# Kernel optimization log

Measured on AMD Instinct MI355X. Metric: run time of the kernel, lower is better.

The kernel has to match this reference:

```python
import jax, jax.numpy as jnp
import numpy as np

B, S, E = 2, 2048, 2048
H, G = 16, 4
HD = E // H          # 128
GD = HD * G          # 512
NGH = H // G         # 4 (tile factor for K/V heads)


def setup_inputs() -> dict:
    key = jax.random.key(0)
    ks = jax.random.split(key, 6)
    sc = 0.02
    return {
        "x": jax.random.normal(ks[0], (B, S, E), dtype=jnp.float32),
        "mask": jnp.ones((B, S, S), dtype=jnp.int32),
        "Wq": jax.random.normal(ks[1], (E, E), dtype=jnp.float32) * sc,
        "bq": jnp.zeros((E,), dtype=jnp.float32),
        "Wk": jax.random.normal(ks[2], (E, GD), dtype=jnp.float32) * sc,
        "bk": jnp.zeros((GD,), dtype=jnp.float32),
        "Wv": jax.random.normal(ks[3], (E, GD), dtype=jnp.float32) * sc,
        "bv": jnp.zeros((GD,), dtype=jnp.float32),
        "Wo": jax.random.normal(ks[4], (E, E), dtype=jnp.float32) * sc,
        "bo": jnp.zeros((E,), dtype=jnp.float32),
    }


def reference(x, mask, Wq, bq, Wk, bk, Wv, bv, Wo, bo):
    b, s, _ = x.shape
    # projections
    q = x @ Wq + bq                                   # [B,S,E]
    k = x @ Wk + bk                                   # [B,S,GD]
    v = x @ Wv + bv                                   # [B,S,GD]
    q = q.reshape(b, s, H, HD).transpose(0, 2, 1, 3)  # [B,H,S,hd]
    k = k.reshape(b, s, G, HD).transpose(0, 2, 1, 3)  # [B,G,S,hd]
    v = v.reshape(b, s, G, HD).transpose(0, 2, 1, 3)
    # torch .repeat(1, NGH, 1, 1): tile groups -> head h uses group h % G
    k = jnp.tile(k, (1, NGH, 1, 1))                   # [B,H,S,hd]
    v = jnp.tile(v, (1, NGH, 1, 1))
    scale = 1.0 / np.sqrt(HD).astype(np.float32)
    scores = jnp.einsum("bhqd,bhkd->bhqk", q, k) * scale
    m = mask[:, None, :, :]                           # [B,1,S,S]
    scores = jnp.where(m == 0, jnp.float32(-10000.0), scores)
    attn = jax.nn.softmax(scores, axis=-1)
    out = jnp.einsum("bhqk,bhkd->bhqd", attn, v)      # [B,H,S,hd]
    out = out.transpose(0, 2, 1, 3).reshape(b, s, E)  # [B,S,E]
    return out @ Wo + bo
```

## Files before the change

kernel.cpp:

```cpp
#include <hip/hip_runtime.h>

#define B_ 2
#define S_ 2048
#define E_ 2048
#define H_ 16
#define G_ 4
#define HD_ 128
#define GD_ 512
#define KVLD_ 1024
#define QKVN_ 3072
#define M_ (B_*S_)

using u16 = unsigned short;
using u32 = unsigned int;
typedef __attribute__((ext_vector_type(8))) short short8;
typedef __attribute__((ext_vector_type(4))) float f32x4;

#define QSCL 0.12751891114f
#define MASKED_L2 (-14427.0f)

__device__ __forceinline__ u16 f2bf(float f) {
  union { float f; unsigned u; } v; v.f = f;
  unsigned r = v.u + 0x7fff + ((v.u >> 16) & 1);
  return (u16)(r >> 16);
}

__device__ __forceinline__ void async16(const void* g, void* l) {
  __builtin_amdgcn_global_load_lds((const __attribute__((address_space(1))) unsigned int*)g,
                                   (__attribute__((address_space(3))) unsigned int*)l, 16, 0, 0);
}

__global__ __launch_bounds__(256) void cast_f32_bf16(const float* __restrict__ in,
                                                     u16* __restrict__ out, int n4) {
  int i = blockIdx.x * 256 + threadIdx.x;
  if (i >= n4) return;
  float4 v = ((const float4*)in)[i];
  union { u16 o[4]; uint2 u; } pk;
  pk.o[0] = f2bf(v.x); pk.o[1] = f2bf(v.y); pk.o[2] = f2bf(v.z); pk.o[3] = f2bf(v.w);
  *(uint2*)(out + (size_t)i * 4) = pk.u;
}

__global__ __launch_bounds__(256) void concat_bias3(const float* __restrict__ a,
                                                    const float* __restrict__ b,
                                                    const float* __restrict__ c,
                                                    float* __restrict__ o) {
  int t = blockIdx.x * 256 + threadIdx.x;
  if (t < 2048) o[t] = a[t];
  else if (t < 2560) o[t] = b[t - 2048];
  else if (t < 3072) o[t] = c[t - 2560];
}

__global__ __launch_bounds__(256) void transpose_cast(const float* __restrict__ W,
                                                      u16* __restrict__ Wt, int K, int N) {
  __shared__ u16 tile[64 * 72];
  int n0 = blockIdx.x * 64, k0 = blockIdx.y * 64;
  int t = threadIdx.x;
  int row = t >> 2;
  int seg = t & 3;
  const float* src = W + (size_t)(k0 + row) * N + n0 + seg * 16;
  #pragma unroll
  for (int i = 0; i < 4; ++i) {
    float4 v = *(const float4*)(src + i * 4);
    int nl = seg * 16 + i * 4;
    tile[(nl + 0) * 72 + row] = f2bf(v.x);
    tile[(nl + 1) * 72 + row] = f2bf(v.y);
    tile[(nl + 2) * 72 + row] = f2bf(v.z);
    tile[(nl + 3) * 72 + row] = f2bf(v.w);
  }
  __syncthreads();
  int nl = t >> 2, s2 = t & 3;
  u16* dst = Wt + (size_t)(n0 + nl) * K + k0 + s2 * 16;
  *(uint4*)dst       = *(const uint4*)&tile[nl * 72 + s2 * 16];
  *(uint4*)(dst + 8) = *(const uint4*)&tile[nl * 72 + s2 * 16 + 8];
}

__global__ __launch_bounds__(256) void transpose_v(const u16* __restrict__ KVb, u16* __restrict__ Vtg) {
  __shared__ u16 tile[64 * 72];
  int kv0 = blockIdx.x * 64;
  int gn0 = blockIdx.y * 64;
  int t = threadIdx.x;
  int row = t >> 2, seg = t & 3;
  int prow = (row & 15) * 4 + (row >> 4);
  const u16* src = KVb + (size_t)(kv0 + row) * KVLD_ + 512 + gn0 + seg * 16;
  union { uint4 v; u16 s[8]; } a, b;
  a.v = *(const uint4*)src; b.v = *(const uint4*)(src + 8);
  #pragma unroll
  for (int j = 0; j < 8; ++j) tile[(seg * 16 + j) * 72 + prow] = a.s[j];
  #pragma unroll
  for (int j = 0; j < 8; ++j) tile[(seg * 16 + 8 + j) * 72 + prow] = b.s[j];
  __syncthreads();
  int gl = t >> 2, ks2 = t & 3;
  int bb = kv0 >> 11;
  int s0 = kv0 & 2047;
  int gn = gn0 + gl;
  u16* dst = Vtg + (size_t)(bb * 512 + gn) * S_ + s0 + ks2 * 16;
  *(uint4*)dst       = *(const uint4*)&tile[gl * 72 + ks2 * 16];
  *(uint4*)(dst + 8) = *(const uint4*)&tile[gl * 72 + ks2 * 16 + 8];
}

__global__ __launch_bounds__(256) void mask_flags(const int* __restrict__ mask, int* __restrict__ flags) {
  int idx = blockIdx.x * 4 + (threadIdx.x >> 6);
  int lane = threadIdx.x & 63;
  int bb = idx >> 12, rg = (idx >> 5) & 127, kt = idx & 31;
  const int* base = mask + ((size_t)bb * S_ + rg * 16) * S_ + kt * 64;
  int row = lane >> 2, c0 = (lane & 3) * 16;
  int ok = 1;
  #pragma unroll
  for (int i = 0; i < 4; ++i) {
    int4 v = *(const int4*)&base[(size_t)row * S_ + c0 + i * 4];
    ok &= (v.x != 0) & (v.y != 0) & (v.z != 0) & (v.w != 0);
  }
  ok = __all(ok) ? 1 : 0;
  if (lane == 0) flags[idx] = ok;
}

__global__ __launch_bounds__(256) void gemm_qkv(const u16* __restrict__ A, const u16* __restrict__ Bt,
                                                const float* __restrict__ bias,
                                                u16* __restrict__ Qb, u16* __restrict__ KVb, int K) {
  __shared__ u16 As[128 * 32];
  __shared__ u16 Bs[128 * 32];
  int nbx = gridDim.x;
  int bid = blockIdx.y * nbx + blockIdx.x;
  int chunk = (nbx * gridDim.y) >> 3;
  int swz = (bid & 7) * chunk + (bid >> 3);
  int n0 = (swz % nbx) * 128, m0 = (swz / nbx) * 128;
  int t = threadIdx.x;
  int w = t >> 6, lane = t & 63, c = lane & 15, q = lane >> 4;
  int wm = w & 1, wn = w >> 1;
  int r0 = t >> 2, kc = t & 3;
  const u16* Ag0 = A  + (size_t)(m0 + r0) * K + kc * 8;
  const u16* Ag1 = A  + (size_t)(m0 + 64 + r0) * K + kc * 8;
  const u16* Bg0 = Bt + (size_t)(n0 + r0) * K + kc * 8;
  const u16* Bg1 = Bt + (size_t)(n0 + 64 + r0) * K + kc * 8;
  f32x4 acc[4][4] = {};
  for (int k0 = 0; k0 < K; k0 += 32) {
    async16(Ag0 + k0, &As[t * 8]);
    async16(Ag1 + k0, &As[2048 + t * 8]);
    async16(Bg0 + k0, &Bs[t * 8]);
    async16(Bg1 + k0, &Bs[2048 + t * 8]);
    __syncthreads();
    short8 af[4], bf[4];
    #pragma unroll
    for (int i = 0; i < 4; ++i) {
      af[i] = *(const short8*)&As[(wm * 64 + i * 16 + c) * 32 + q * 8];
      bf[i] = *(const short8*)&Bs[(wn * 64 + i * 16 + c) * 32 + q * 8];
    }
    #pragma unroll
    for (int i = 0; i < 4; ++i)
      #pragma unroll
      for (int j = 0; j < 4; ++j)
        acc[i][j] = __builtin_amdgcn_mfma_f32_16x16x32_bf16(af[i], bf[j], acc[i][j], 0, 0, 0);
    __syncthreads();
  }
  int isq = (n0 < 2048);
  #pragma unroll
  for (int i = 0; i < 4; ++i) {
    int mrow_base = m0 + wm * 64 + i * 16 + q * 4;
    #pragma unroll
    for (int j = 0; j < 4; ++j) {
      int coln = n0 + wn * 64 + j * 16 + c;
      float bv = bias[coln];
      #pragma unroll
      for (int r = 0; r < 4; ++r) {
        float v = acc[i][j][r] + bv;
        if (isq) Qb[(size_t)(mrow_base + r) * E_ + coln] = f2bf(v * QSCL);
        else     KVb[(size_t)(mrow_base + r) * KVLD_ + coln - 2048] = f2bf(v);
      }
    }
  }
}

__global__ __launch_bounds__(256) void gemm_k(const u16* __restrict__ A, const u16* __restrict__ Bt,
                                              const float* __restrict__ bias, float* __restrict__ Cout,
                                              int M, int N, int K) {
  __shared__ u16 As[128 * 32];
  __shared__ u16 Bs[128 * 32];
  int nbx = gridDim.x;
  int bid = blockIdx.y * nbx + blockIdx.x;
  int chunk = (nbx * gridDim.y) >> 3;
  int swz = (bid & 7) * chunk + (bid >> 3);
  int n0 = (swz % nbx) * 128, m0 = (swz / nbx) * 128;
  int t = threadIdx.x;
  int w = t >> 6, lane = t & 63, c = lane & 15, q = lane >> 4;
  int wm = w & 1, wn = w >> 1;
  int r0 = t >> 2, kc = t & 3;
  const u16* Ag0 = A  + (size_t)(m0 + r0) * K + kc * 8;
  const u16* Ag1 = A  + (size_t)(m0 + 64 + r0) * K + kc * 8;
  const u16* Bg0 = Bt + (size_t)(n0 + r0) * K + kc * 8;
  const u16* Bg1 = Bt + (size_t)(n0 + 64 + r0) * K + kc * 8;
  f32x4 acc[4][4] = {};
  for (int k0 = 0; k0 < K; k0 += 32) {
    async16(Ag0 + k0, &As[t * 8]);
    async16(Ag1 + k0, &As[2048 + t * 8]);
    async16(Bg0 + k0, &Bs[t * 8]);
    async16(Bg1 + k0, &Bs[2048 + t * 8]);
    __syncthreads();
    short8 af[4], bf[4];
    #pragma unroll
    for (int i = 0; i < 4; ++i) {
      af[i] = *(const short8*)&As[(wm * 64 + i * 16 + c) * 32 + q * 8];
      bf[i] = *(const short8*)&Bs[(wn * 64 + i * 16 + c) * 32 + q * 8];
    }
    #pragma unroll
    for (int i = 0; i < 4; ++i)
      #pragma unroll
      for (int j = 0; j < 4; ++j)
        acc[i][j] = __builtin_amdgcn_mfma_f32_16x16x32_bf16(af[i], bf[j], acc[i][j], 0, 0, 0);
    __syncthreads();
  }
  #pragma unroll
  for (int i = 0; i < 4; ++i) {
    int mrow_base = m0 + wm * 64 + i * 16 + q * 4;
    #pragma unroll
    for (int j = 0; j < 4; ++j) {
      int coln = n0 + wn * 64 + j * 16 + c;
      float bv = bias[coln];
      #pragma unroll
      for (int r = 0; r < 4; ++r)
        Cout[(size_t)(mrow_base + r) * N + coln] = acc[i][j][r] + bv;
    }
  }
}

__global__ __launch_bounds__(512) void attn_k(const u16* __restrict__ Q, const u16* __restrict__ KVb,
                                              const u16* __restrict__ Vtg, const int* __restrict__ mask,
                                              const int* __restrict__ mflags, u16* __restrict__ O) {
  __shared__ u16 Ks[2][64 * 128];
  __shared__ u16 Vs[2][128 * 64];
  __shared__ u16 Ps[8 * 16 * 64];
  int bid = blockIdx.x;
  int mt = bid & 15, h = (bid >> 4) & 15, bb = bid >> 8;
  int g = h & 3;
  int t = threadIdx.x, w = t >> 6, lane = t & 63, c = lane & 15, q = lane >> 4;
  int m0 = mt * 128;

  const u16* Qbase  = Q   + (size_t)(bb * S_ + m0) * E_ + h * HD_;
  const u16* Kbase  = KVb + (size_t)bb * S_ * KVLD_ + g * HD_;
  const u16* Vtbase = Vtg + (size_t)(bb * G_ + g) * HD_ * S_;

  int krow0 = t >> 4;
  int kkc   = ((t & 15) ^ (krow0 & 15)) * 8;
  const u16* Kst = Kbase + (size_t)krow0 * KVLD_ + kkc;
  int vn0 = t >> 3;
  int vkc = ((t & 7) ^ (vn0 & 7)) * 8;
  const u16* Vst = Vtbase + (size_t)vn0 * S_ + vkc;

  int pwa[4], pra[2];
  #pragma unroll
  for (int r = 0; r < 4; ++r) {
    int row = q * 4 + r;
    pwa[r] = w * 1024 + row * 64 + (((c >> 1) ^ (row & 7)) * 8) + (c & 1) * 4;
  }
  #pragma unroll
  for (int ks = 0; ks < 2; ++ks)
    pra[ks] = w * 1024 + c * 64 + (((ks * 4 + q) ^ (c & 7)) * 8);

  short8 aq[4];
  #pragma unroll
  for (int k0 = 0; k0 < 4; ++k0)
    aq[k0] = *(const short8*)&Qbase[(size_t)(w * 16 + c) * E_ + k0 * 32 + q * 8];

  const short8 ones = {(short)0x3F80, (short)0x3F80, (short)0x3F80, (short)0x3F80,
                       (short)0x3F80, (short)0x3F80, (short)0x3F80, (short)0x3F80};

  f32x4 Oa[8] = {};
  f32x4 lacc = {};

  #pragma unroll
  for (int p = 0; p < 2; ++p)
    async16(Kst + (size_t)(p * 32) * KVLD_, &Ks[0][p * 4096 + t * 8]);
  #pragma unroll
  for (int p = 0; p < 2; ++p)
    async16(Vst + (size_t)(p * 64) * S_, &Vs[0][p * 4096 + t * 8]);

  for (int kv0 = 0; kv0 < S_; kv0 += 64) {
    int cur = (kv0 >> 6) & 1;
    __syncthreads();
    if (kv0 + 64 < S_) {
      #pragma unroll
      for (int p = 0; p < 2; ++p)
        async16(Kst + (size_t)(kv0 + 64 + p * 32) * KVLD_, &Ks[cur ^ 1][p * 4096 + t * 8]);
      #pragma unroll
      for (int p = 0; p < 2; ++p)
        async16(Vst + (size_t)(p * 64) * S_ + kv0 + 64, &Vs[cur ^ 1][p * 4096 + t * 8]);
    }
    const u16* K_ = Ks[cur];
    const u16* V_ = Vs[cur];

    f32x4 sc[4] = {};
    #pragma unroll
    for (int k0 = 0; k0 < 4; ++k0) {
      short8 bk[4];
      #pragma unroll
      for (int ns = 0; ns < 4; ++ns)
        bk[ns] = *(const short8*)&K_[(ns * 16 + c) * 128 + (((k0 * 4 + q) ^ c) * 8)];
      #pragma unroll
      for (int ns = 0; ns < 4; ++ns)
        sc[ns] = __builtin_amdgcn_mfma_f32_16x16x32_bf16(aq[k0], bk[ns], sc[ns], 0, 0, 0);
    }
    {
      int flag = mflags[bb * 4096 + (mt * 8 + w) * 32 + (kv0 >> 6)];
      if (!flag) {
        #pragma unroll
        for (int r = 0; r < 4; ++r) {
          int qrow = m0 + w * 16 + q * 4 + r;
          const int* mrow = mask + ((size_t)bb * S_ + qrow) * S_ + kv0;
          #pragma unroll
          for (int ns = 0; ns < 4; ++ns)
            if (mrow[ns * 16 + c] == 0) sc[ns][r] = MASKED_L2;
        }
      }
    }
    #pragma unroll
    for (int r = 0; r < 4; ++r) {
      u32 u[4];
      #pragma unroll
      for (int ns = 0; ns < 4; ++ns) {
        float p = __builtin_amdgcn_exp2f(sc[ns][r]);
        u[ns] = __float_as_uint(p) + 0x8000u;
      }
      uint2 pk;
      pk.x = __builtin_amdgcn_perm(u[1], u[0], 0x07060302);
      pk.y = __builtin_amdgcn_perm(u[3], u[2], 0x07060302);
      *(uint2*)&Ps[pwa[r]] = pk;
    }
    __asm__ volatile("" ::: "memory");
    #pragma unroll
    for (int ks = 0; ks < 2; ++ks) {
      short8 ap = *(const short8*)&Ps[pra[ks]];
      lacc = __builtin_amdgcn_mfma_f32_16x16x32_bf16(ap, ones, lacc, 0, 0, 0);
      #pragma unroll
      for (int d = 0; d < 8; ++d) {
        short8 bv = *(const short8*)&V_[(d * 16 + c) * 64 + (((ks * 4 + q) ^ (c & 7)) * 8)];
        Oa[d] = __builtin_amdgcn_mfma_f32_16x16x32_bf16(ap, bv, Oa[d], 0, 0, 0);
      }
    }
  }
  {
    float inv[4];
    #pragma unroll
    for (int r = 0; r < 4; ++r) inv[r] = 1.0f / lacc[r];
    #pragma unroll
    for (int d = 0; d < 8; ++d)
      #pragma unroll
      for (int r = 0; r < 4; ++r) {
        size_t off = (size_t)(bb * S_ + m0 + w * 16 + q * 4 + r) * E_ + h * HD_ + d * 16 + c;
        O[off] = f2bf(Oa[d][r] * inv[r]);
      }
  }
}

extern "C" void kernel_launch(void* const* d_in, const int* in_sizes, int n_in,
                              void* d_out, int out_size, void* d_ws, size_t ws_size,
                              hipStream_t stream) {
  const float* x    = (const float*)d_in[0];
  const int*   mask = (const int*)d_in[1];
  const float* Wq   = (const float*)d_in[2];
  const float* bq   = (const float*)d_in[3];
  const float* Wk   = (const float*)d_in[4];
  const float* bk   = (const float*)d_in[5];
  const float* Wv   = (const float*)d_in[6];
  const float* bv   = (const float*)d_in[7];
  const float* Wo   = (const float*)d_in[8];
  const float* bo   = (const float*)d_in[9];
  float* out = (float*)d_out;

  char* ws = (char*)d_ws;
  u16* xb    = (u16*)ws; ws += (size_t)M_ * E_ * 2;
  u16* Wqkvt = (u16*)ws; ws += (size_t)QKVN_ * E_ * 2;
  u16* Wot   = (u16*)ws; ws += (size_t)E_ * E_ * 2;
  u16* Qb    = (u16*)ws; ws += (size_t)M_ * E_ * 2;
  u16* KVb   = (u16*)ws; ws += (size_t)M_ * KVLD_ * 2;
  u16* Ob    = (u16*)ws; ws += (size_t)M_ * E_ * 2;
  u16* Vtg   = (u16*)ws; ws += (size_t)B_ * G_ * HD_ * S_ * 2;
  int* mfl   = (int*)ws; ws += (size_t)B_ * 128 * 32 * 4;
  float* bqkv = (float*)ws; ws += QKVN_ * 4;

  cast_f32_bf16<<<(M_ * E_ / 4 + 255) / 256, 256, 0, stream>>>(x, xb, M_ * E_ / 4);
  transpose_cast<<<dim3(E_ / 64,  E_ / 64), 256, 0, stream>>>(Wq, Wqkvt, E_, E_);
  transpose_cast<<<dim3(GD_ / 64, E_ / 64), 256, 0, stream>>>(Wk, Wqkvt + (size_t)2048 * E_, E_, GD_);
  transpose_cast<<<dim3(GD_ / 64, E_ / 64), 256, 0, stream>>>(Wv, Wqkvt + (size_t)2560 * E_, E_, GD_);
  transpose_cast<<<dim3(E_ / 64,  E_ / 64), 256, 0, stream>>>(Wo, Wot, E_, E_);
  concat_bias3<<<QKVN_ / 256, 256, 0, stream>>>(bq, bk, bv, bqkv);
  mask_flags<<<B_ * 128 * 32 / 4, 256, 0, stream>>>(mask, mfl);

  gemm_qkv<<<dim3(QKVN_ / 128, M_ / 128), 256, 0, stream>>>(xb, Wqkvt, bqkv, Qb, KVb, E_);
  transpose_v<<<dim3(M_ / 64, GD_ / 64), 256, 0, stream>>>(KVb, Vtg);

  attn_k<<<B_ * H_ * (S_ / 128), 512, 0, stream>>>(Qb, KVb, Vtg, mask, mfl, Ob);

  gemm_k<<<dim3(E_ / 128, M_ / 128), 256, 0, stream>>>(Ob, Wot, bo, out, M_, E_, E_);
}
```

Baseline: 362.8 us.

## Double-buffer LDS tiles and XOR-swizzle chunks in both GEMM kernels

Both the QKV projection GEMM and the output GEMM now use two LDS buffers. The next K-slice is prefetched asynchronously while MFMAs run on the current one, and the second barrier per iteration is dropped. The 16-byte chunk layout within each LDS row is also XOR-swizzled by row, on both the store and the read side, to cut bank conflicts on the fragment loads. This doubles LDS use per block, which could reduce occupancy, and the overlap depends on how the async copies are waited on at the barrier.

```diff
diff --git a/kernel.cpp b/kernel.cpp
--- a/kernel.cpp
+++ b/kernel.cpp
@@ -117,8 +117,8 @@
 __global__ __launch_bounds__(256) void gemm_qkv(const u16* __restrict__ A, const u16* __restrict__ Bt,
                                                 const float* __restrict__ bias,
                                                 u16* __restrict__ Qb, u16* __restrict__ KVb, int K) {
-  __shared__ u16 As[128 * 32];
-  __shared__ u16 Bs[128 * 32];
+  __shared__ u16 As[2][128 * 32];
+  __shared__ u16 Bs[2][128 * 32];
   int nbx = gridDim.x;
   int bid = blockIdx.y * nbx + blockIdx.x;
   int chunk = (nbx * gridDim.y) >> 3;
@@ -127,30 +127,38 @@
   int t = threadIdx.x;
   int w = t >> 6, lane = t & 63, c = lane & 15, q = lane >> 4;
   int wm = w & 1, wn = w >> 1;
-  int r0 = t >> 2, kc = t & 3;
-  const u16* Ag0 = A  + (size_t)(m0 + r0) * K + kc * 8;
-  const u16* Ag1 = A  + (size_t)(m0 + 64 + r0) * K + kc * 8;
-  const u16* Bg0 = Bt + (size_t)(n0 + r0) * K + kc * 8;
-  const u16* Bg1 = Bt + (size_t)(n0 + 64 + r0) * K + kc * 8;
+  int r0 = t >> 2;
+  int kcs = ((t & 3) ^ ((t >> 3) & 3)) * 8;
+  const u16* Ag0 = A  + (size_t)(m0 + r0) * K + kcs;
+  const u16* Ag1 = A  + (size_t)(m0 + 64 + r0) * K + kcs;
+  const u16* Bg0 = Bt + (size_t)(n0 + r0) * K + kcs;
+  const u16* Bg1 = Bt + (size_t)(n0 + 64 + r0) * K + kcs;
+  int roff = (q ^ ((c >> 1) & 3)) * 8;
   f32x4 acc[4][4] = {};
+  async16(Ag0, &As[0][t * 8]);
+  async16(Ag1, &As[0][2048 + t * 8]);
+  async16(Bg0, &Bs[0][t * 8]);
+  async16(Bg1, &Bs[0][2048 + t * 8]);
   for (int k0 = 0; k0 < K; k0 += 32) {
-    async16(Ag0 + k0, &As[t * 8]);
-    async16(Ag1 + k0, &As[2048 + t * 8]);
-    async16(Bg0 + k0, &Bs[t * 8]);
-    async16(Bg1 + k0, &Bs[2048 + t * 8]);
+    int cur = (k0 >> 5) & 1;
     __syncthreads();
+    if (k0 + 32 < K) {
+      async16(Ag0 + k0 + 32, &As[cur ^ 1][t * 8]);
+      async16(Ag1 + k0 + 32, &As[cur ^ 1][2048 + t * 8]);
+      async16(Bg0 + k0 + 32, &Bs[cur ^ 1][t * 8]);
+      async16(Bg1 + k0 + 32, &Bs[cur ^ 1][2048 + t * 8]);
+    }
     short8 af[4], bf[4];
     #pragma unroll
     for (int i = 0; i < 4; ++i) {
-      af[i] = *(const short8*)&As[(wm * 64 + i * 16 + c) * 32 + q * 8];
-      bf[i] = *(const short8*)&Bs[(wn * 64 + i * 16 + c) * 32 + q * 8];
+      af[i] = *(const short8*)&As[cur][(wm * 64 + i * 16 + c) * 32 + roff];
+      bf[i] = *(const short8*)&Bs[cur][(wn * 64 + i * 16 + c) * 32 + roff];
     }
     #pragma unroll
     for (int i = 0; i < 4; ++i)
       #pragma unroll
       for (int j = 0; j < 4; ++j)
         acc[i][j] = __builtin_amdgcn_mfma_f32_16x16x32_bf16(af[i], bf[j], acc[i][j], 0, 0, 0);
-    __syncthreads();
   }
   int isq = (n0 < 2048);
   #pragma unroll
@@ -173,8 +181,8 @@
 __global__ __launch_bounds__(256) void gemm_k(const u16* __restrict__ A, const u16* __restrict__ Bt,
                                               const float* __restrict__ bias, float* __restrict__ Cout,
                                               int M, int N, int K) {
-  __shared__ u16 As[128 * 32];
-  __shared__ u16 Bs[128 * 32];
+  __shared__ u16 As[2][128 * 32];
+  __shared__ u16 Bs[2][128 * 32];
   int nbx = gridDim.x;
   int bid = blockIdx.y * nbx + blockIdx.x;
   int chunk = (nbx * gridDim.y) >> 3;
@@ -183,30 +191,38 @@
   int t = threadIdx.x;
   int w = t >> 6, lane = t & 63, c = lane & 15, q = lane >> 4;
   int wm = w & 1, wn = w >> 1;
-  int r0 = t >> 2, kc = t & 3;
-  const u16* Ag0 = A  + (size_t)(m0 + r0) * K + kc * 8;
-  const u16* Ag1 = A  + (size_t)(m0 + 64 + r0) * K + kc * 8;
-  const u16* Bg0 = Bt + (size_t)(n0 + r0) * K + kc * 8;
-  const u16* Bg1 = Bt + (size_t)(n0 + 64 + r0) * K + kc * 8;
+  int r0 = t >> 2;
+  int kcs = ((t & 3) ^ ((t >> 3) & 3)) * 8;
+  const u16* Ag0 = A  + (size_t)(m0 + r0) * K + kcs;
+  const u16* Ag1 = A  + (size_t)(m0 + 64 + r0) * K + kcs;
+  const u16* Bg0 = Bt + (size_t)(n0 + r0) * K + kcs;
+  const u16* Bg1 = Bt + (size_t)(n0 + 64 + r0) * K + kcs;
+  int roff = (q ^ ((c >> 1) & 3)) * 8;
   f32x4 acc[4][4] = {};
+  async16(Ag0, &As[0][t * 8]);
+  async16(Ag1, &As[0][2048 + t * 8]);
+  async16(Bg0, &Bs[0][t * 8]);
+  async16(Bg1, &Bs[0][2048 + t * 8]);
   for (int k0 = 0; k0 < K; k0 += 32) {
-    async16(Ag0 + k0, &As[t * 8]);
-    async16(Ag1 + k0, &As[2048 + t * 8]);
-    async16(Bg0 + k0, &Bs[t * 8]);
-    async16(Bg1 + k0, &Bs[2048 + t * 8]);
+    int cur = (k0 >> 5) & 1;
     __syncthreads();
+    if (k0 + 32 < K) {
+      async16(Ag0 + k0 + 32, &As[cur ^ 1][t * 8]);
+      async16(Ag1 + k0 + 32, &As[cur ^ 1][2048 + t * 8]);
+      async16(Bg0 + k0 + 32, &Bs[cur ^ 1][t * 8]);
+      async16(Bg1 + k0 + 32, &Bs[cur ^ 1][2048 + t * 8]);
+    }
     short8 af[4], bf[4];
     #pragma unroll
     for (int i = 0; i < 4; ++i) {
-      af[i] = *(const short8*)&As[(wm * 64 + i * 16 + c) * 32 + q * 8];
-      bf[i] = *(const short8*)&Bs[(wn * 64 + i * 16 + c) * 32 + q * 8];
+      af[i] = *(const short8*)&As[cur][(wm * 64 + i * 16 + c) * 32 + roff];
+      bf[i] = *(const short8*)&Bs[cur][(wn * 64 + i * 16 + c) * 32 + roff];
     }
     #pragma unroll
     for (int i = 0; i < 4; ++i)
       #pragma unroll
       for (int j = 0; j < 4; ++j)
         acc[i][j] = __builtin_amdgcn_mfma_f32_16x16x32_bf16(af[i], bf[j], acc[i][j], 0, 0, 0);
-    __syncthreads();
   }
   #pragma unroll
   for (int i = 0; i < 4; ++i) {
```

Result: faster. 351.2 us (-3.2%).
